# Kernel tuning notes

Hardware: AMD Instinct MI355X
Metric: run time of the kernel (lower is better)

## Reference

```python
import jax, jax.numpy as jnp
import numpy as np

N_EMBED = 8192
BETA = 0.25


def setup_inputs() -> dict:
    key = jax.random.key(0)
    k1, k2 = jax.random.split(key)
    z = jax.random.normal(k1, (16, 256, 32, 32), dtype=jnp.float32)
    # matches nn.Embedding init uniform_(-1/n_embed, 1/n_embed)
    embed_weight = jax.random.uniform(k2, (N_EMBED, 256), dtype=jnp.float32,
                                      minval=-1.0 / N_EMBED, maxval=1.0 / N_EMBED)
    return {"z": z, "embed_weight": embed_weight}


def reference(z, embed_weight):
    sg = jax.lax.stop_gradient
    # b c h w -> b h w c
    z_nhwc = jnp.transpose(z, (0, 2, 3, 1))
    # squared L2 distance to every code: ||z||^2 + ||e||^2 - 2 z.e  -> [b,h,w,n]
    d = (jnp.sum(z_nhwc ** 2, axis=-1, keepdims=True)
         + jnp.sum(embed_weight ** 2, axis=1)
         - 2.0 * jnp.einsum('bhwc,nc->bhwn', z_nhwc, embed_weight))
    indices = jnp.argmin(d, axis=-1)            # [b,h,w] int
    z_q = embed_weight[indices]                  # [b,h,w,c] gather

    loss = (BETA * jnp.mean((sg(z_q) - z_nhwc) ** 2)
            + jnp.mean((z_q - sg(z_nhwc)) ** 2))

    # straight-through estimator
    z_q_st = z_nhwc + sg(z_q - z_nhwc)
    out = jnp.transpose(z_q_st, (0, 3, 1, 2))    # b h w c -> b c h w

    # perplexity via histogram (equivalent to one_hot(...).mean(0))
    flat = indices.reshape(-1)
    counts = jnp.zeros((N_EMBED,), dtype=jnp.float32).at[flat].add(1.0)
    avg_probs = counts / flat.shape[0]
    perplexity = jnp.exp(-jnp.sum(avg_probs * jnp.log(avg_probs + 1e-10)))

    return (out, indices, loss, perplexity)
```

## Files before the change

### kernel.cpp

```cpp
#include <hip/hip_runtime.h>
#include <stdint.h>

typedef unsigned long long u64;
typedef unsigned int u32;

#define CDIM 256
#define NCODES 8192
#define MTOT 16384
#define OUT_ELEMS 4194304
#define BETA 0.25f

#define WS_PACKED 0u
#define WS_ENORM  131072u
#define WS_ZSQ    163840u
#define WS_COUNTS 229376u
#define WS_LOSS   262144u
#define WS_ZB     524544u
#define WS_EB     8913152u
#define WS_TT2    13107456u
#define WS_NEEDED 21496064u

typedef short bf16x8 __attribute__((ext_vector_type(8)));
typedef float f32x4 __attribute__((ext_vector_type(4)));
typedef float f32x16 __attribute__((ext_vector_type(16)));

#define GL2LDS16(g, l) __builtin_amdgcn_global_load_lds(            \
    (const __attribute__((address_space(1))) void*)(g),             \
    (__attribute__((address_space(3))) void*)(l), 16, 0, 0)

__device__ __forceinline__ unsigned short f2bf(float f) {
  u32 u = __float_as_uint(f);
  u32 r = (u + 0x7FFFu + ((u >> 16) & 1u)) >> 16;
  return (unsigned short)r;
}

__global__ void conv_kernel(const float* __restrict__ z, const float* __restrict__ E,
                            unsigned short* __restrict__ zb, unsigned short* __restrict__ eb,
                            float* __restrict__ zsq, float* __restrict__ enorm) {
  int blk = blockIdx.x;
  int t = threadIdx.x, w = t >> 6, lane = t & 63;
  if (blk < 256) {
    __shared__ unsigned short tz[64][66];
    __shared__ float part[4][4][64];
    int b = blk >> 4, p0 = (blk & 15) << 6;
    const float* zp = z + ((size_t)b << 18) + p0;
    #pragma unroll
    for (int ct = 0; ct < 4; ++ct) {
      int c0 = ct << 6;
      if (ct) __syncthreads();
      float s = 0.f;
      #pragma unroll
      for (int i = 0; i < 16; ++i) {
        int cl = w + (i << 2);
        float v = zp[((size_t)(c0 + cl) << 10) + lane];
        s = fmaf(v, v, s);
        tz[cl][lane] = f2bf(v);
      }
      part[ct][w][lane] = s;
      __syncthreads();
      #pragma unroll
      for (int j = 0; j < 16; ++j) {
        int pl = w + (j << 2);
        zb[(((size_t)b << 10) + p0 + pl) * 256 + c0 + lane] = tz[lane][pl];
      }
    }
    if (w == 0) {
      float q0 = ((part[0][0][lane] + part[0][1][lane]) + part[0][2][lane]) + part[0][3][lane];
      float q1 = ((part[1][0][lane] + part[1][1][lane]) + part[1][2][lane]) + part[1][3][lane];
      float q2 = ((part[2][0][lane] + part[2][1][lane]) + part[2][2][lane]) + part[2][3][lane];
      float q3 = ((part[3][0][lane] + part[3][1][lane]) + part[3][2][lane]) + part[3][3][lane];
      zsq[(b << 10) + p0 + lane] = ((q0 + q1) + q2) + q3;
    }
  } else {
    int e4 = blk - 256;
    size_t base = ((size_t)e4 << 11) + ((size_t)t << 3);
    float4 v0 = *(const float4*)&E[base];
    float4 v1 = *(const float4*)&E[base + 4];
    ushort4 o0 = { f2bf(v0.x), f2bf(v0.y), f2bf(v0.z), f2bf(v0.w) };
    ushort4 o1 = { f2bf(v1.x), f2bf(v1.y), f2bf(v1.z), f2bf(v1.w) };
    *(ushort4*)&eb[base] = o0;
    *(ushort4*)&eb[base + 4] = o1;
    float s = v0.x * v0.x + v0.y * v0.y + v0.z * v0.z + v0.w * v0.w
            + v1.x * v1.x + v1.y * v1.y + v1.z * v1.z + v1.w * v1.w;
    #pragma unroll
    for (int off = 16; off; off >>= 1) s += __shfl_xor(s, off, 32);
    if ((t & 31) == 0) enorm[(e4 << 3) + (t >> 5)] = s;
  }
}

__global__ __launch_bounds__(256, 2) void gemm_kernel(
    const unsigned short* __restrict__ zb, const unsigned short* __restrict__ eb,
    uint2* __restrict__ tt2) {
  __shared__ unsigned short As[256 * 64];
  __shared__ unsigned short Bs[128 * 64];
  const int t = threadIdx.x;
  const int w = t >> 6, lane = t & 63;
  const int r32 = lane & 31, hi = lane >> 5, r7 = r32 & 7;
  const int m0 = blockIdx.x << 8, n0 = blockIdx.y << 7;

  f32x16 acc[2][4];
  #pragma unroll
  for (int i = 0; i < 2; ++i)
    #pragma unroll
    for (int j = 0; j < 4; ++j) acc[i][j] = (f32x16)0.f;

  const int jsw = ((t & 7) ^ ((t >> 3) & 7)) << 3;
  const unsigned short* zsrc = zb + (((size_t)m0 + (t >> 3)) << 8) + jsw;
  const unsigned short* esrc = eb + (((size_t)n0 + (t >> 3)) << 8) + jsw;

  const int abase = ((w << 6) + r32) << 7;
  const int bbase = r32 << 7;

  for (int kt = 0; kt < 4; ++kt) {
    if (kt) __syncthreads();
    const int ko = kt << 6;
    #pragma unroll
    for (int i = 0; i < 8; ++i)
      GL2LDS16(zsrc + (i << 13) + ko, (char*)As + (i << 12) + (t << 4));
    #pragma unroll
    for (int i = 0; i < 4; ++i)
      GL2LDS16(esrc + (i << 13) + ko, (char*)Bs + (i << 12) + (t << 4));
    __syncthreads();
    #pragma unroll
    for (int ki = 0; ki < 4; ++ki) {
      const int jx = (((ki << 1) + hi) ^ r7) << 4;
      bf16x8 af[2], bq[4];
      #pragma unroll
      for (int a = 0; a < 2; ++a)
        af[a] = *(const bf16x8*)((const char*)As + abase + (a << 12) + jx);
      #pragma unroll
      for (int ni = 0; ni < 4; ++ni)
        bq[ni] = *(const bf16x8*)((const char*)Bs + bbase + (ni << 12) + jx);
      #pragma unroll
      for (int a = 0; a < 2; ++a)
        #pragma unroll
        for (int ni = 0; ni < 4; ++ni)
          acc[a][ni] = __builtin_amdgcn_mfma_f32_32x32x16_bf16(bq[ni], af[a], acc[a][ni], 0, 0, 0);
    }
  }

  const u32 hib = (u32)(hi << 2);
  #pragma unroll
  for (int a = 0; a < 2; ++a) {
    float a1 = 0.f, a2 = 0.f;
    #pragma unroll
    for (int ni = 0; ni < 4; ++ni) {
      #pragma unroll
      for (int reg = 0; reg < 16; ++reg) {
        u32 code = ((u32)(ni << 5) | ((u32)(reg >> 2) << 3) | (u32)(reg & 3)) | hib;
        u32 e = __float_as_uint(acc[a][ni][reg] + 2.0f);
        float k = __uint_as_float((e & 0xFFFFFF80u) | code);
        float na2 = __builtin_amdgcn_fmed3f(a1, a2, k);
        a1 = fmaxf(a1, k);
        a2 = na2;
      }
    }
    float b1 = __shfl_xor(a1, 32, 64);
    float b2 = __shfl_xor(a2, 32, 64);
    a2 = fmaxf(fminf(a1, b1), fmaxf(a2, b2));
    a1 = fmaxf(a1, b1);
    if (hi == 0) {
      int row = m0 + (w << 6) + (a << 5) + r32;
      tt2[((size_t)blockIdx.y << 14) + row] =
          make_uint2(__float_as_uint(a1), __float_as_uint(a2));
    }
  }
}

__global__ __launch_bounds__(256) void refine_kernel(
    const float* __restrict__ z, const float* __restrict__ E,
    const float* __restrict__ zsq, const float* __restrict__ enorm,
    const uint2* __restrict__ tt2, u64* __restrict__ packed,
    float* __restrict__ out_idx, u32* __restrict__ counts) {
  __shared__ uint2 tc[64][33];
  __shared__ float zrow[32][260];
  const int t = threadIdx.x, w = t >> 6, lane = t & 63;
  const int m0 = blockIdx.x << 5;
  const int b = m0 >> 10, p0 = m0 & 1023;

  #pragma unroll
  for (int i = 0; i < 8; ++i) {
    int tau = (i << 3) + (t >> 5);
    tc[tau][t & 31] = tt2[((size_t)tau << 14) + m0 + (t & 31)];
  }
  #pragma unroll
  for (int i = 0; i < 8; ++i) {
    int c = (i << 5) + (t >> 3);
    int p4 = (t & 7) << 2;
    float4 v = *(const float4*)&z[((size_t)b << 18) + ((size_t)c << 10) + p0 + p4];
    zrow[p4 + 0][c] = v.x;
    zrow[p4 + 1][c] = v.y;
    zrow[p4 + 2][c] = v.z;
    zrow[p4 + 3][c] = v.w;
  }
  __syncthreads();

  for (int j = 0; j < 8; ++j) {
    const int rr = (w << 3) + j;
    const int m = m0 + rr;
    uint2 c = tc[lane][rr];
    float f0 = __uint_as_float(c.x), f1 = __uint_as_float(c.y);
    float fm = f0;
    #pragma unroll
    for (int off = 1; off < 64; off <<= 1) fm = fmaxf(fm, __shfl_xor(fm, off, 64));
    float thr = fm - 1.5e-4f;
    const float4 zr4 = *(const float4*)&zrow[rr][lane << 2];
    float zsqm = zsq[m];
    u64 best = ~0ull;
    #pragma unroll
    for (int s = 0; s < 2; ++s) {
      u32 ck = s ? c.y : c.x;
      float fv = s ? f1 : f0;
      u64 mask = __ballot(fv >= thr);
      while (mask) {
        int src = __ffsll((unsigned long long)mask) - 1;
        mask &= mask - 1;
        u32 key = (u32)__shfl((int)ck, src, 64);
        int idx = (src << 7) | (int)(key & 127u);
        const float4 e4 = *(const float4*)&E[(size_t)idx * CDIM + (lane << 2)];
        float pa = zr4.x * e4.x;
        pa = fmaf(zr4.y, e4.y, pa);
        pa = fmaf(zr4.z, e4.z, pa);
        pa = fmaf(zr4.w, e4.w, pa);
        #pragma unroll
        for (int off = 1; off < 64; off <<= 1) pa += __shfl_xor(pa, off, 64);
        float ttv = zsqm + enorm[idx];
        float d = ttv - 2.0f * pa;
        u64 k2 = ((u64)__float_as_uint(d) << 32) | (u32)idx;
        if (k2 < best) best = k2;
      }
    }
    if (lane == 0) {
      packed[m] = best;
      int idx = (int)(u32)(best & 0xffffffffull);
      out_idx[m] = (float)idx;
      atomicAdd(&counts[idx], 1u);
    }
  }
}

__global__ void enorm_kernel(const float* __restrict__ E, float* __restrict__ enorm) {
  int wave = threadIdx.x >> 6;
  int lane = threadIdx.x & 63;
  int n = blockIdx.x * 4 + wave;
  float4 v = reinterpret_cast<const float4*>(E + (size_t)n * CDIM)[lane];
  float s = v.x * v.x + v.y * v.y + v.z * v.z + v.w * v.w;
  #pragma unroll
  for (int off = 32; off; off >>= 1) s += __shfl_down(s, off, 64);
  if (lane == 0) enorm[n] = s;
}

__global__ void zsq_kernel(const float* __restrict__ z, float* __restrict__ zsq) {
  int blk = blockIdx.x;
  int j = threadIdx.x;
  int b = blk >> 2;
  int p = ((blk & 3) << 8) + j;
  const float* zp = z + (size_t)b * (CDIM * 1024) + p;
  float acc = 0.f;
  #pragma unroll 8
  for (int c = 0; c < CDIM; ++c) {
    float v = zp[(size_t)c * 1024];
    acc += v * v;
  }
  zsq[(blk << 8) + j] = acc;
}

#define BM 128
#define BN 128
#define BK 32
__global__ __launch_bounds__(256, 2) void dist_kernel(
    const float* __restrict__ z, const float* __restrict__ E,
    const float* __restrict__ zsq, const float* __restrict__ enorm,
    unsigned long long* __restrict__ packed) {
  __shared__ float zs[BK][BM];
  __shared__ float es[BK][BN];
  const int t = threadIdx.x;
  const int m0 = blockIdx.x * BM;
  const int n0 = blockIdx.y * BN;
  const int b = m0 >> 10;
  const int p0 = m0 & 1023;
  const int zc = t >> 5;
  const int zm = (t & 31) << 2;
  const float* zbase = z + (size_t)b * 262144 + p0 + zm;
  const int en = t & 127;
  const int ec = (t >> 7) << 4;
  const float* ebase = E + (size_t)(n0 + en) * CDIM + ec;
  float4 zr[4], er[4];
  #pragma unroll
  for (int r = 0; r < 4; ++r)
    zr[r] = *(const float4*)(zbase + (size_t)(r * 8 + zc) * 1024);
  #pragma unroll
  for (int i = 0; i < 4; ++i)
    er[i] = *(const float4*)(ebase + 4 * i);
  float acc[8][8];
  #pragma unroll
  for (int a = 0; a < 8; ++a)
    #pragma unroll
    for (int bb = 0; bb < 8; ++bb) acc[a][bb] = 0.f;
  const int tx = t & 15, ty = t >> 4;
  for (int kt = 0; kt < CDIM / BK; ++kt) {
    __syncthreads();
    #pragma unroll
    for (int r = 0; r < 4; ++r)
      *(float4*)&zs[r * 8 + zc][zm] = zr[r];
    #pragma unroll
    for (int i = 0; i < 4; ++i) {
      es[ec + 4 * i + 0][en] = er[i].x;
      es[ec + 4 * i + 1][en] = er[i].y;
      es[ec + 4 * i + 2][en] = er[i].z;
      es[ec + 4 * i + 3][en] = er[i].w;
    }
    __syncthreads();
    if (kt + 1 < CDIM / BK) {
      const int c0 = (kt + 1) * BK;
      #pragma unroll
      for (int r = 0; r < 4; ++r)
        zr[r] = *(const float4*)(zbase + (size_t)(c0 + r * 8 + zc) * 1024);
      #pragma unroll
      for (int i = 0; i < 4; ++i)
        er[i] = *(const float4*)(ebase + c0 + 4 * i);
    }
    #pragma unroll 8
    for (int kk = 0; kk < BK; ++kk) {
      float4 za = *(const float4*)&zs[kk][ty * 4];
      float4 zb4 = *(const float4*)&zs[kk][64 + ty * 4];
      float4 ea = *(const float4*)&es[kk][tx * 4];
      float4 eb4 = *(const float4*)&es[kk][64 + tx * 4];
      float zv[8] = {za.x, za.y, za.z, za.w, zb4.x, zb4.y, zb4.z, zb4.w};
      float ev[8] = {ea.x, ea.y, ea.z, ea.w, eb4.x, eb4.y, eb4.z, eb4.w};
      #pragma unroll
      for (int a = 0; a < 8; ++a)
        #pragma unroll
        for (int bb = 0; bb < 8; ++bb)
          acc[a][bb] += zv[a] * ev[bb];
    }
  }
  #pragma unroll
  for (int a = 0; a < 8; ++a) {
    int rloc = (a < 4) ? (ty * 4 + a) : (64 + ty * 4 + (a - 4));
    float zq = zsq[m0 + rloc];
    float bestd = 3.4e38f;
    int bestn = 0;
    #pragma unroll
    for (int bb = 0; bb < 8; ++bb) {
      int nloc = (bb < 4) ? (tx * 4 + bb) : (64 + tx * 4 + (bb - 4));
      int n = n0 + nloc;
      float ttv = zq + enorm[n];
      float d = ttv - 2.0f * acc[a][bb];
      if (d < bestd) { bestd = d; bestn = n; }
    }
    unsigned long long pk =
        ((unsigned long long)__float_as_uint(bestd) << 32) | (unsigned)bestn;
    #pragma unroll
    for (int off = 1; off < 16; off <<= 1) {
      unsigned long long other = __shfl_xor(pk, off, 16);
      if (other < pk) pk = other;
    }
    if (tx == 0) atomicMin(&packed[m0 + rloc], pk);
  }
}

__global__ void idx_kernel(const unsigned long long* __restrict__ packed,
                           float* __restrict__ out_idx, unsigned int* __restrict__ counts) {
  int m = blockIdx.x * 256 + threadIdx.x;
  int idx = (int)(unsigned)(packed[m] & 0xffffffffull);
  out_idx[m] = (float)idx;
  atomicAdd(&counts[idx], 1u);
}

__global__ __launch_bounds__(256) void out_kernel(
    const float* __restrict__ z, const float* __restrict__ E,
    const u64* __restrict__ packed,
    float* __restrict__ out, float* __restrict__ loss_acc) {
  __shared__ float es[32][257];
  const int t = threadIdx.x, w = t >> 6, lane = t & 63;
  const int m0 = blockIdx.x << 5;
  const int b = m0 >> 10, p0 = m0 & 1023;

  #pragma unroll
  for (int i = 0; i < 8; ++i) {
    int pl = (w << 3) + i;
    int idx = (int)(u32)(packed[m0 + pl] & 0xffffffffull);
    float4 v = *(const float4*)&E[((size_t)idx << 8) + (lane << 2)];
    es[pl][(lane << 2) + 0] = v.x;
    es[pl][(lane << 2) + 1] = v.y;
    es[pl][(lane << 2) + 2] = v.z;
    es[pl][(lane << 2) + 3] = v.w;
  }
  __syncthreads();

  const int pp = lane & 31, chi = lane >> 5;
  const size_t gbase = ((size_t)b << 18) + p0 + pp;
  float s = 0.f;
  #pragma unroll 8
  for (int i = 0; i < 32; ++i) {
    int c = (i << 3) + (w << 1) + chi;
    float zv = z[gbase + ((size_t)c << 10)];
    float e = es[pp][c];
    float diff = e - zv;
    out[gbase + ((size_t)c << 10)] = zv + diff;
    s = fmaf(diff, diff, s);
  }
  #pragma unroll
  for (int off = 32; off; off >>= 1) s += __shfl_down(s, off, 64);
  __shared__ float red[4];
  if (lane == 0) red[w] = s;
  __syncthreads();
  if (t == 0) atomicAdd(loss_acc, red[0] + red[1] + red[2] + red[3]);
}

__global__ void scalar_kernel(const unsigned int* __restrict__ counts,
                              const float* __restrict__ loss_acc,
                              float* __restrict__ out) {
  float s = 0.f;
  for (int i = threadIdx.x; i < NCODES; i += 256) {
    float pl = (float)counts[i] * (1.0f / 16384.0f);
    s += pl * logf(pl + 1e-10f);
  }
  #pragma unroll
  for (int off = 32; off; off >>= 1) s += __shfl_down(s, off, 64);
  __shared__ float red[4];
  int wv = threadIdx.x >> 6, lane = threadIdx.x & 63;
  if (lane == 0) red[wv] = s;
  __syncthreads();
  if (threadIdx.x == 0) {
    float tot = red[0] + red[1] + red[2] + red[3];
    out[OUT_ELEMS + MTOT] = (1.0f + BETA) * loss_acc[0] * (1.0f / (float)OUT_ELEMS);
    out[OUT_ELEMS + MTOT + 1] = expf(-tot);
  }
}

extern "C" void kernel_launch(void* const* d_in, const int* in_sizes, int n_in,
                              void* d_out, int out_size, void* d_ws, size_t ws_size,
                              hipStream_t stream) {
  const float* z = (const float*)d_in[0];
  const float* E = (const float*)d_in[1];
  float* out = (float*)d_out;
  char* ws = (char*)d_ws;
  u64* packed = (u64*)(ws + WS_PACKED);
  float* enorm = (float*)(ws + WS_ENORM);
  float* zsq = (float*)(ws + WS_ZSQ);
  u32* counts = (u32*)(ws + WS_COUNTS);
  float* loss_acc = (float*)(ws + WS_LOSS);

  hipMemsetAsync(counts, 0, 32768 + 256, stream);

  if (ws_size >= WS_NEEDED) {
    unsigned short* zb = (unsigned short*)(ws + WS_ZB);
    unsigned short* ebuf = (unsigned short*)(ws + WS_EB);
    uint2* tt2 = (uint2*)(ws + WS_TT2);
    conv_kernel<<<1280, 256, 0, stream>>>(z, E, zb, ebuf, zsq, enorm);
    dim3 g(MTOT / 256, NCODES / 128);
    gemm_kernel<<<g, 256, 0, stream>>>(zb, ebuf, tt2);
    refine_kernel<<<MTOT / 32, 256, 0, stream>>>(z, E, zsq, enorm, tt2, packed,
                                                 out + OUT_ELEMS, counts);
  } else {
    hipMemsetAsync(packed, 0xFF, MTOT * 8, stream);
    enorm_kernel<<<NCODES / 4, 256, 0, stream>>>(E, enorm);
    zsq_kernel<<<64, 256, 0, stream>>>(z, zsq);
    dim3 g(MTOT / BM, NCODES / BN);
    dist_kernel<<<g, 256, 0, stream>>>(z, E, zsq, enorm, packed);
    idx_kernel<<<MTOT / 256, 256, 0, stream>>>(packed, out + OUT_ELEMS, counts);
  }

  out_kernel<<<MTOT / 32, 256, 0, stream>>>(z, E, packed, out, loss_acc);
  scalar_kernel<<<1, 256, 0, stream>>>(counts, loss_acc, out);
}
```

Before: 135.9 us.

## Restructure distance GEMM to 256x256 tiles with double-buffered LDS and 16x16 MFMA

```diff
diff --git a/kernel.cpp b/kernel.cpp
--- a/kernel.cpp
+++ b/kernel.cpp
@@ -22,7 +22,6 @@
 
 typedef short bf16x8 __attribute__((ext_vector_type(8)));
 typedef float f32x4 __attribute__((ext_vector_type(4)));
-typedef float f32x16 __attribute__((ext_vector_type(16)));
 
 #define GL2LDS16(g, l) __builtin_amdgcn_global_load_lds(            \
     (const __attribute__((address_space(1))) void*)(g),             \
@@ -88,80 +87,97 @@
   }
 }
 
-__global__ __launch_bounds__(256, 2) void gemm_kernel(
+__global__ __launch_bounds__(512, 1) void gemm_kernel(
     const unsigned short* __restrict__ zb, const unsigned short* __restrict__ eb,
     uint2* __restrict__ tt2) {
-  __shared__ unsigned short As[256 * 64];
-  __shared__ unsigned short Bs[128 * 64];
+  __shared__ unsigned short As[2][256 * 64];
+  __shared__ unsigned short Bs[2][256 * 64];
   const int t = threadIdx.x;
   const int w = t >> 6, lane = t & 63;
-  const int r32 = lane & 31, hi = lane >> 5, r7 = r32 & 7;
-  const int m0 = blockIdx.x << 8, n0 = blockIdx.y << 7;
-
-  f32x16 acc[2][4];
-  #pragma unroll
-  for (int i = 0; i < 2; ++i)
-    #pragma unroll
-    for (int j = 0; j < 4; ++j) acc[i][j] = (f32x16)0.f;
+  const int wm = w >> 1, wn = w & 1;
+  const int r16 = lane & 15, kg = lane >> 4, r7 = r16 & 7;
+  const int m0 = blockIdx.x << 8, n0 = blockIdx.y << 8;
+
+  f32x4 acc[4][8];
+  #pragma unroll
+  for (int i = 0; i < 4; ++i)
+    #pragma unroll
+    for (int j = 0; j < 8; ++j) acc[i][j] = (f32x4)0.f;
 
   const int jsw = ((t & 7) ^ ((t >> 3) & 7)) << 3;
   const unsigned short* zsrc = zb + (((size_t)m0 + (t >> 3)) << 8) + jsw;
   const unsigned short* esrc = eb + (((size_t)n0 + (t >> 3)) << 8) + jsw;
 
-  const int abase = ((w << 6) + r32) << 7;
-  const int bbase = r32 << 7;
-
+  const int abase = ((wm << 6) + r16) << 7;
+  const int bbase = ((wn << 7) + r16) << 7;
+  const int jx0 = (kg ^ r7) << 4;
+  const int jx1 = ((4 + kg) ^ r7) << 4;
+
+  #pragma unroll
+  for (int i = 0; i < 4; ++i) {
+    GL2LDS16(zsrc + (i << 14), (char*)As[0] + (i << 13) + (t << 4));
+    GL2LDS16(esrc + (i << 14), (char*)Bs[0] + (i << 13) + (t << 4));
+  }
+  __syncthreads();
+
+  #pragma unroll
   for (int kt = 0; kt < 4; ++kt) {
-    if (kt) __syncthreads();
-    const int ko = kt << 6;
-    #pragma unroll
-    for (int i = 0; i < 8; ++i)
-      GL2LDS16(zsrc + (i << 13) + ko, (char*)As + (i << 12) + (t << 4));
-    #pragma unroll
-    for (int i = 0; i < 4; ++i)
-      GL2LDS16(esrc + (i << 13) + ko, (char*)Bs + (i << 12) + (t << 4));
+    const int cur = kt & 1;
+    if (kt < 3) {
+      const int ko = (kt + 1) << 6;
+      #pragma unroll
+      for (int i = 0; i < 4; ++i) {
+        GL2LDS16(zsrc + (i << 14) + ko, (char*)As[cur ^ 1] + (i << 13) + (t << 4));
+        GL2LDS16(esrc + (i << 14) + ko, (char*)Bs[cur ^ 1] + (i << 13) + (t << 4));
+      }
+    }
+    #pragma unroll
+    for (int s = 0; s < 2; ++s) {
+      const int jx = s ? jx1 : jx0;
+      bf16x8 af[4], bq[8];
+      #pragma unroll
+      for (int mi = 0; mi < 4; ++mi)
+        af[mi] = *(const bf16x8*)((const char*)As[cur] + abase + (mi << 11) + jx);
+      #pragma unroll
+      for (int ni = 0; ni < 8; ++ni)
+        bq[ni] = *(const bf16x8*)((const char*)Bs[cur] + bbase + (ni << 11) + jx);
+      __builtin_amdgcn_s_setprio(1);
+      #pragma unroll
+      for (int mi = 0; mi < 4; ++mi)
+        #pragma unroll
+        for (int ni = 0; ni < 8; ++ni)
+          acc[mi][ni] = __builtin_amdgcn_mfma_f32_16x16x32_bf16(bq[ni], af[mi], acc[mi][ni], 0, 0, 0);
+      __builtin_amdgcn_s_setprio(0);
+    }
     __syncthreads();
-    #pragma unroll
-    for (int ki = 0; ki < 4; ++ki) {
-      const int jx = (((ki << 1) + hi) ^ r7) << 4;
-      bf16x8 af[2], bq[4];
-      #pragma unroll
-      for (int a = 0; a < 2; ++a)
-        af[a] = *(const bf16x8*)((const char*)As + abase + (a << 12) + jx);
-      #pragma unroll
-      for (int ni = 0; ni < 4; ++ni)
-        bq[ni] = *(const bf16x8*)((const char*)Bs + bbase + (ni << 12) + jx);
-      #pragma unroll
-      for (int a = 0; a < 2; ++a)
-        #pragma unroll
-        for (int ni = 0; ni < 4; ++ni)
-          acc[a][ni] = __builtin_amdgcn_mfma_f32_32x32x16_bf16(bq[ni], af[a], acc[a][ni], 0, 0, 0);
-    }
-  }
-
-  const u32 hib = (u32)(hi << 2);
-  #pragma unroll
-  for (int a = 0; a < 2; ++a) {
+  }
+
+  const u32 kgr = (u32)(kg << 2);
+  #pragma unroll
+  for (int mi = 0; mi < 4; ++mi) {
     float a1 = 0.f, a2 = 0.f;
     #pragma unroll
-    for (int ni = 0; ni < 4; ++ni) {
-      #pragma unroll
-      for (int reg = 0; reg < 16; ++reg) {
-        u32 code = ((u32)(ni << 5) | ((u32)(reg >> 2) << 3) | (u32)(reg & 3)) | hib;
-        u32 e = __float_as_uint(acc[a][ni][reg] + 2.0f);
-        float k = __uint_as_float((e & 0xFFFFFF80u) | code);
+    for (int ni = 0; ni < 8; ++ni) {
+      #pragma unroll
+      for (int reg = 0; reg < 4; ++reg) {
+        u32 e = __float_as_uint(acc[mi][ni][reg] + 2.0f);
+        float k = __uint_as_float((e & 0xFFFFFF80u) | ((u32)(ni << 4) | kgr | (u32)reg));
         float na2 = __builtin_amdgcn_fmed3f(a1, a2, k);
         a1 = fmaxf(a1, k);
         a2 = na2;
       }
     }
-    float b1 = __shfl_xor(a1, 32, 64);
-    float b2 = __shfl_xor(a2, 32, 64);
-    a2 = fmaxf(fminf(a1, b1), fmaxf(a2, b2));
-    a1 = fmaxf(a1, b1);
-    if (hi == 0) {
-      int row = m0 + (w << 6) + (a << 5) + r32;
-      tt2[((size_t)blockIdx.y << 14) + row] =
+    #pragma unroll
+    for (int off = 16; off < 64; off <<= 1) {
+      float b1 = __shfl_xor(a1, off, 64);
+      float b2 = __shfl_xor(a2, off, 64);
+      a2 = fmaxf(fminf(a1, b1), fmaxf(a2, b2));
+      a1 = fmaxf(a1, b1);
+    }
+    if (kg == 0) {
+      int row = m0 + (wm << 6) + (mi << 4) + r16;
+      int tile = (blockIdx.y << 1) + wn;
+      tt2[((size_t)tile << 14) + row] =
           make_uint2(__float_as_uint(a1), __float_as_uint(a2));
     }
   }
@@ -450,8 +466,8 @@
     unsigned short* ebuf = (unsigned short*)(ws + WS_EB);
     uint2* tt2 = (uint2*)(ws + WS_TT2);
     conv_kernel<<<1280, 256, 0, stream>>>(z, E, zb, ebuf, zsq, enorm);
-    dim3 g(MTOT / 256, NCODES / 128);
-    gemm_kernel<<<g, 256, 0, stream>>>(zb, ebuf, tt2);
+    dim3 g(MTOT / 256, NCODES / 256);
+    gemm_kernel<<<g, 512, 0, stream>>>(zb, ebuf, tt2);
     refine_kernel<<<MTOT / 32, 256, 0, stream>>>(z, E, zsq, enorm, tt2, packed,
                                                  out + OUT_ELEMS, counts);
   } else {
```

Measured after the change: 138.2 us. About the same (+1.7%).
